# Optimization experiments

Measured on AMD Instinct MI355X. Metric: run time of the kernel, lower is better.

## Reference

```python
import jax, jax.numpy as jnp
import numpy as np

PS = 16            # patch size
STEP = PS - 2      # stride (overlap of 2)
HEADS = 4
DIM = 64
QK = 64
MLP = 128

def _grid(h):
    # static (numpy) row indices of all patch pixels, matching patch_divide's loop
    starts = np.arange(0, h + STEP - PS, STEP)
    tops = np.minimum(starts + PS, h) - PS
    return (tops[:, None] + np.arange(PS)).ravel(), len(starts)

def _div_mask(h):
    # rows/cols covered by two patches get divided by 2 (patch_reverse loops)
    m = np.ones(h, np.float32)
    for i in range(STEP, h + STEP - PS, STEP):
        d = min(i + PS - STEP, h)
        if i < d:
            m[i:d] = 2.0
    return m

def _layernorm(x, g, b):
    mu = x.mean(-1, keepdims=True)
    var = ((x - mu) ** 2).mean(-1, keepdims=True)
    return (x - mu) * jax.lax.rsqrt(var + 1e-5) * g + b

def setup_inputs() -> dict:
    key = jax.random.key(0)
    ks = jax.random.split(key, 8)
    f = lambda k, shp: jax.random.normal(k, shp, jnp.float32) * 0.05
    return {
        "x": jax.random.normal(ks[0], (2, DIM, 226, 226), jnp.float32),
        "ln1_g": jnp.ones((DIM,), jnp.float32), "ln1_b": jnp.zeros((DIM,), jnp.float32),
        "wq": f(ks[1], (DIM, QK)), "wk": f(ks[2], (DIM, QK)), "wv": f(ks[3], (DIM, DIM)),
        "w_proj": f(ks[4], (DIM, DIM)), "b_proj": jnp.zeros((DIM,), jnp.float32),
        "ln2_g": jnp.ones((DIM,), jnp.float32), "ln2_b": jnp.zeros((DIM,), jnp.float32),
        "w_fc1": f(ks[5], (DIM, MLP)), "b_fc1": jnp.zeros((MLP,), jnp.float32),
        "w_dw": f(ks[6], (MLP, 1, 5, 5)), "b_dw": jnp.zeros((MLP,), jnp.float32),
        "w_fc2": f(ks[7], (MLP, DIM)), "b_fc2": jnp.zeros((DIM,), jnp.float32),
    }

def reference(x, ln1_g, ln1_b, wq, wk, wv, w_proj, b_proj,
              ln2_g, ln2_b, w_fc1, b_fc1, w_dw, b_dw, w_fc2, b_fc2):
    b, c, h, w = x.shape
    ri, nh = _grid(h)
    ci, nw = _grid(w)
    n = nh * nw
    # --- patch_divide (vectorized gather of overlapping windows) ---
    p = x[:, :, ri][:, :, :, ci].reshape(b, c, nh, PS, nw, PS)
    t = p.transpose(0, 2, 4, 3, 5, 1).reshape(b * n, PS * PS, c)  # (b n)(h w)c
    # --- PreNorm attention (SDPA default scale = head_dim**-0.5) ---
    y = _layernorm(t, ln1_g, ln1_b)
    dh = QK // HEADS
    q = (y @ wq).reshape(-1, PS * PS, HEADS, dh)
    k = (y @ wk).reshape(-1, PS * PS, HEADS, dh)
    v = (y @ wv).reshape(-1, PS * PS, HEADS, DIM // HEADS)
    logits = jnp.einsum('bqhd,bkhd->bhqk', q, k) * (dh ** -0.5)
    a = jax.nn.softmax(logits, axis=-1)
    o = jnp.einsum('bhqk,bkhd->bqhd', a, v).reshape(-1, PS * PS, DIM)
    t = (o @ w_proj + b_proj) + t
    # --- PreNorm ConvFFN ---
    y = _layernorm(t, ln2_g, ln2_b)
    y = jax.nn.gelu(y @ w_fc1 + b_fc1, approximate=False)
    img = y.reshape(-1, PS, PS, MLP).transpose(0, 3, 1, 2)  # NCHW
    dw = jax.lax.conv_general_dilated(
        img, w_dw, (1, 1), [(2, 2), (2, 2)],
        feature_group_count=MLP,
        dimension_numbers=('NCHW', 'OIHW', 'NCHW')) + b_dw[None, :, None, None]
    dw = jax.nn.gelu(dw, approximate=False).transpose(0, 2, 3, 1).reshape(y.shape)
    y = y + dw
    t = (y @ w_fc2 + b_fc2) + t
    # --- patch_reverse (overlap-add scatter + averaging of double-covered bands) ---
    vals = t.reshape(b, nh, nw, PS, PS, c).transpose(0, 5, 1, 3, 2, 4).reshape(b, c, -1)
    idx = (ri[:, None] * w + ci[None, :]).ravel()
    out = jnp.zeros((b, c, h * w), x.dtype).at[:, :, idx].add(vals)
    out = out.reshape(b, c, h, w) / (_div_mask(h)[:, None] * _div_mask(w)[None, :])
    return out
```

## Files before the change

kernel.cpp:

```cpp
#include <hip/hip_runtime.h>
#include <hip/hip_bf16.h>
#include <math.h>

#define HH 226
#define WW 226
#define HWIMG (226*226)
#define PS 16
#define STP 14
#define TOK 256
#define NPATCH 512
#define NTOK (NPATCH*TOK)
#define OUT_ELEMS (2*64*226*226)

typedef unsigned int u32;
typedef unsigned short u16;
typedef __attribute__((ext_vector_type(8))) short short8;
typedef __attribute__((ext_vector_type(4))) float f32x4;

__device__ __forceinline__ float lo16(u32 u){ return __uint_as_float(u << 16); }
__device__ __forceinline__ float hi16(u32 u){ return __uint_as_float(u & 0xFFFF0000u); }
__device__ __forceinline__ u16 f2bf(float f){
    u32 u = __float_as_uint(f);
    u += 0x7FFFu + ((u >> 16) & 1u);
    return (u16)(u >> 16);
}
__device__ __forceinline__ u32 pack2(float a, float b){
#if defined(__gfx950__) && __has_builtin(__builtin_amdgcn_cvt_pk_bf16_f32)
    auto r = __builtin_amdgcn_cvt_pk_bf16_f32(a, b);
    return *(u32*)&r;
#else
    return (u32)f2bf(a) | ((u32)f2bf(b) << 16);
#endif
}
__device__ __forceinline__ float fexp2(float x){
#if __has_builtin(__builtin_amdgcn_exp2f)
    return __builtin_amdgcn_exp2f(x);
#else
    return exp2f(x);
#endif
}
__device__ __forceinline__ void unpack8(uint4 r, float* d){
    d[0]=lo16(r.x); d[1]=hi16(r.x); d[2]=lo16(r.y); d[3]=hi16(r.y);
    d[4]=lo16(r.z); d[5]=hi16(r.z); d[6]=lo16(r.w); d[7]=hi16(r.w);
}
__device__ __forceinline__ uint4 pack8(const float* a){
    uint4 uu;
    uu.x = pack2(a[0], a[1]);
    uu.y = pack2(a[2], a[3]);
    uu.z = pack2(a[4], a[5]);
    uu.w = pack2(a[6], a[7]);
    return uu;
}
__device__ __forceinline__ float gelu_f(float x){
    return 0.5f * x * (1.0f + erff(x * 0.70710678118654752f));
}

template<int N>
__device__ __forceinline__ void store_bf16(u32* dst, const float* a){
    uint4* p4 = (uint4*)(dst);
    #pragma unroll
    for (int w4 = 0; w4 < N/8; ++w4) p4[w4] = pack8(a + 8*w4);
}

__global__ __launch_bounds__(256, 4) void k0_wt(
    const float* __restrict__ wq, const float* __restrict__ wk,
    const float* __restrict__ wv, u16* __restrict__ wt)
{
    const int i = blockIdx.x*256 + threadIdx.x;
    const int m = i >> 12, rem = i & 4095;
    const int kk = rem >> 6, n = rem & 63;
    const float* w = (m==0 ? wq : (m==1 ? wk : wv));
    wt[m*4096 + n*64 + kk] = f2bf(w[kk*64 + n]);
}

__global__ __launch_bounds__(512, 4) void k1_qkv(
    const float* __restrict__ x, const float* __restrict__ g1, const float* __restrict__ b1,
    const u16* __restrict__ wt,
    float* __restrict__ t_out, u32* __restrict__ qo, u32* __restrict__ ko, u32* __restrict__ vo)
{
    __shared__ u16 ys[256*72];
    __shared__ u32 strip[8][16*34];
    __shared__ float g_s[64], b_s[64];
    const int tid = threadIdx.x;
    if (tid < 64){ g_s[tid]=g1[tid]; b_s[tid]=b1[tid]; }

    const int p = blockIdx.x;
    const int bi = p >> 8, ph = (p >> 4) & 15, pw = p & 15;

    const int tok = tid >> 1, h = tid & 1;
    const int ti = tok >> 4, tj = tok & 15;
    const int r = ph*STP + ti, c = pw*STP + tj;
    const float* xb = x + ((size_t)bi*64 + 32*h)*HWIMG + (size_t)r*WW + c;
    const size_t gtokA = (size_t)p*TOK + tok;
    float* tp = t_out + gtokA*64 + 32*h;

    float v32[32];
    float s1 = 0.f, s2 = 0.f;
    #pragma unroll
    for (int c8 = 0; c8 < 4; ++c8){
        #pragma unroll
        for (int u = 0; u < 8; ++u){
            const float vv = xb[(size_t)(c8*8+u)*HWIMG];
            v32[c8*8+u] = vv;
            s1 += vv; s2 += vv*vv;
        }
        ((float4*)tp)[c8*2]   = make_float4(v32[c8*8+0],v32[c8*8+1],v32[c8*8+2],v32[c8*8+3]);
        ((float4*)tp)[c8*2+1] = make_float4(v32[c8*8+4],v32[c8*8+5],v32[c8*8+6],v32[c8*8+7]);
    }
    s1 += __shfl_xor(s1, 1);
    s2 += __shfl_xor(s2, 1);
    const float mu = s1 * (1.f/64.f);
    const float var = s2 * (1.f/64.f) - mu*mu;
    const float rs = rsqrtf(var + 1e-5f);
    __syncthreads();
    u32* ysw = (u32*)ys;
    #pragma unroll
    for (int i2 = 0; i2 < 16; ++i2){
        const int kk = 32*h + 2*i2;
        const float a0 = (v32[2*i2]  -mu)*rs*g_s[kk]   + b_s[kk];
        const float a1 = (v32[2*i2+1]-mu)*rs*g_s[kk+1] + b_s[kk+1];
        ysw[tok*36 + 16*h + i2] = pack2(a0, a1);
    }
    __syncthreads();

    const int lane = tid & 63;
    const int w8   = tid >> 6;
    const int c15  = lane & 15;
    const int quad = lane >> 4;
    u32* stw = strip[w8];
    const size_t ptok = (size_t)p * TOK;

    for (int mt = 0; mt < 2; ++mt){
        const int T = w8*32 + mt*16;
        short8 af[2];
        #pragma unroll
        for (int kb = 0; kb < 2; ++kb)
            af[kb] = *(const short8*)(ys + (T + c15)*72 + kb*32 + quad*8);

        #pragma unroll
        for (int m = 0; m < 3; ++m){
            short8 bf[2][4];
            #pragma unroll
            for (int kb = 0; kb < 2; ++kb)
                #pragma unroll
                for (int nt = 0; nt < 4; ++nt)
                    bf[kb][nt] = *(const short8*)(wt + m*4096 + (nt*16 + c15)*64 + kb*32 + quad*8);

            f32x4 C[4];
            #pragma unroll
            for (int nt = 0; nt < 4; ++nt) C[nt] = (f32x4){0.f,0.f,0.f,0.f};
            #pragma unroll
            for (int kb = 0; kb < 2; ++kb)
                #pragma unroll
                for (int nt = 0; nt < 4; ++nt)
                    C[nt] = __builtin_amdgcn_mfma_f32_16x16x32_bf16(af[kb], bf[kb][nt], C[nt], 0, 0, 0);

            if (m == 0){
                #pragma unroll
                for (int nt = 0; nt < 4; ++nt)
                    #pragma unroll
                    for (int rr = 0; rr < 4; ++rr)
                        C[nt][rr] *= 0.3606737602222409f;
            }

            #pragma unroll
            for (int nt = 0; nt < 4; ++nt){
                #pragma unroll
                for (int r2 = 0; r2 < 2; ++r2){
                    const float pv0 = __shfl_xor(C[nt][2*r2],   1);
                    const float pv1 = __shfl_xor(C[nt][2*r2+1], 1);
                    u32 wrd; int row;
                    if ((lane & 1) == 0){ wrd = pack2(C[nt][2*r2], pv0);  row = quad*4 + 2*r2; }
                    else                { wrd = pack2(pv1, C[nt][2*r2+1]); row = quad*4 + 2*r2 + 1; }
                    stw[row*34 + nt*8 + (c15 >> 1)] = wrd;
                }
            }

            u32* om = (m==0 ? qo : (m==1 ? ko : vo));
            #pragma unroll
            for (int i = 0; i < 8; ++i){
                const int flat = i*64 + lane;
                const u32 wv = stw[(flat >> 5)*34 + (flat & 31)];
                om[(ptok + T)*32 + flat] = wv;
            }
        }
    }
}

__global__ __launch_bounds__(256, 2) void k2_attn(
    const u16* __restrict__ qg, const u16* __restrict__ kg,
    const u16* __restrict__ vg, u16* __restrict__ og)
{
    __shared__ u16 plds[4][16*280];
    const int tid  = threadIdx.x;
    const int lane = tid & 63;
    const int h    = tid >> 6;
    const int pb   = blockIdx.x;
    const int p    = pb >> 1;
    const int half = pb & 1;
    const int c15  = lane & 15;
    const int quad = lane >> 4;
    const size_t pbase = (size_t)p * TOK * 64;

    short8 kf[16];
    #pragma unroll
    for (int t = 0; t < 16; ++t){
        short8 bf = {0,0,0,0,0,0,0,0};
        if (quad < 2)
            bf = *(const short8*)(kg + pbase + (size_t)(t*16 + c15)*64 + h*16 + quad*8);
        kf[t] = bf;
    }
    short8 vf[8];
    #pragma unroll
    for (int kb = 0; kb < 8; ++kb){
        #pragma unroll
        for (int j = 0; j < 8; ++j)
            vf[kb][j] = (short)vg[pbase + (size_t)(kb*32 + quad*8 + j)*64 + h*16 + c15];
    }
    u16* pw  = &plds[h][0];
    u32* pwq = (u32*)pw + c15*140;

    for (int qi = 0; qi < 8; ++qi){
        const int qt = half*8 + qi;

        short8 qf = {0,0,0,0,0,0,0,0};
        if (quad < 2)
            qf = *(const short8*)(qg + pbase + (size_t)(qt*16 + c15)*64 + h*16 + quad*8);

        f32x4 St[16];
        #pragma unroll
        for (int t = 0; t < 16; ++t){
            f32x4 z = {0.f,0.f,0.f,0.f};
            St[t] = __builtin_amdgcn_mfma_f32_16x16x32_bf16(kf[t], qf, z, 0, 0, 0);
        }

        float rsm[4] = {0.f,0.f,0.f,0.f};
        #pragma unroll
        for (int t = 0; t < 16; ++t){
            #pragma unroll
            for (int r = 0; r < 4; ++r){
                const float pe = fexp2(St[t][r]);
                St[t][r] = pe;
                rsm[r] += pe;
            }
        }
        float s = (rsm[0]+rsm[1]) + (rsm[2]+rsm[3]);
        s += __shfl_xor(s, 16);
        s += __shfl_xor(s, 32);
        const float rinv = __builtin_amdgcn_rcpf(s);
        float rv[4];
        #pragma unroll
        for (int r = 0; r < 4; ++r) rv[r] = __shfl(rinv, quad*4 + r);

        #pragma unroll
        for (int t = 0; t < 16; ++t){
            uint2 wr;
            wr.x = pack2(St[t][0], St[t][1]);
            wr.y = pack2(St[t][2], St[t][3]);
            *(uint2*)(pwq + t*8 + quad*2) = wr;
        }

        f32x4 O0 = {0.f,0.f,0.f,0.f}, O1 = {0.f,0.f,0.f,0.f};
        #pragma unroll
        for (int kb = 0; kb < 4; ++kb){
            const short8 a0 = *(const short8*)(pw + c15*280 + (2*kb)*32 + quad*8);
            const short8 a1 = *(const short8*)(pw + c15*280 + (2*kb+1)*32 + quad*8);
            O0 = __builtin_amdgcn_mfma_f32_16x16x32_bf16(a0, vf[2*kb],   O0, 0, 0, 0);
            O1 = __builtin_amdgcn_mfma_f32_16x16x32_bf16(a1, vf[2*kb+1], O1, 0, 0, 0);
        }

        #pragma unroll
        for (int r = 0; r < 4; ++r){
            const float ov = (O0[r] + O1[r]) * rv[r];
            og[pbase + (size_t)(qt*16 + quad*4 + r)*64 + h*16 + c15] = f2bf(ov);
        }
    }
}

__global__ __launch_bounds__(256, 2) void k3_proj_fc1(
    const u16* __restrict__ og, float* __restrict__ t,
    const float* __restrict__ wp, const float* __restrict__ bp,
    const float* __restrict__ g2, const float* __restrict__ b2,
    const float* __restrict__ wf1, const float* __restrict__ bf1,
    u32* __restrict__ y3)
{
    __shared__ u16 strip[4][16*136];
    __shared__ float bp_s[64], g_s[64], b_s[64], bf_s[128];
    const int tid  = threadIdx.x;
    const int lane = tid & 63;
    const int w    = tid >> 6;
    const int c15  = lane & 15;
    const int quad = lane >> 4;
    if (tid < 64){ bp_s[tid]=bp[tid]; g_s[tid]=g2[tid]; b_s[tid]=b2[tid]; }
    else if (tid >= 128){ const int j = tid - 128; bf_s[j] = bf1[j]; }
    __syncthreads();

    short8 wpf[2][4];
    short8 wff[2][8];
    #pragma unroll
    for (int kb = 0; kb < 2; ++kb){
        #pragma unroll
        for (int nt = 0; nt < 4; ++nt){
            #pragma unroll
            for (int j = 0; j < 8; ++j)
                wpf[kb][nt][j] = (short)f2bf(wp[(kb*32 + quad*8 + j)*64 + nt*16 + c15]);
        }
        #pragma unroll
        for (int nt = 0; nt < 8; ++nt){
            #pragma unroll
            for (int j = 0; j < 8; ++j)
                wff[kb][nt][j] = (short)f2bf(wf1[(kb*32 + quad*8 + j)*128 + nt*16 + c15]);
        }
    }

    const int p = blockIdx.x;
    const size_t pbase = (size_t)p * TOK;
    u16* st = strip[w];
    u32* stw = (u32*)st;

    const float gch[4] = { g_s[0*16+c15], g_s[1*16+c15], g_s[2*16+c15], g_s[3*16+c15] };
    const float bch[4] = { b_s[0*16+c15], b_s[1*16+c15], b_s[2*16+c15], b_s[3*16+c15] };
    const float bpc[4] = { bp_s[0*16+c15], bp_s[1*16+c15], bp_s[2*16+c15], bp_s[3*16+c15] };

    for (int rt = 0; rt < 4; ++rt){
        const int T = w*64 + rt*16;

        short8 af[2];
        #pragma unroll
        for (int kb = 0; kb < 2; ++kb)
            af[kb] = *(const short8*)(og + (pbase + T + c15)*64 + kb*32 + quad*8);

        f32x4 C[4];
        #pragma unroll
        for (int nt = 0; nt < 4; ++nt){
            const float b = bpc[nt];
            C[nt] = (f32x4){b, b, b, b};
        }
        #pragma unroll
        for (int kb = 0; kb < 2; ++kb)
            #pragma unroll
            for (int nt = 0; nt < 4; ++nt)
                C[nt] = __builtin_amdgcn_mfma_f32_16x16x32_bf16(af[kb], wpf[kb][nt], C[nt], 0, 0, 0);

        #pragma unroll
        for (int nt = 0; nt < 4; ++nt){
            #pragma unroll
            for (int r = 0; r < 4; ++r)
                C[nt][r] += t[(pbase + T + quad*4 + r)*64 + nt*16 + c15];
        }
        #pragma unroll
        for (int nt = 0; nt < 4; ++nt){
            #pragma unroll
            for (int r = 0; r < 4; ++r)
                t[(pbase + T + quad*4 + r)*64 + nt*16 + c15] = C[nt][r];
        }

        float rs1[4] = {0,0,0,0}, rs2[4] = {0,0,0,0};
        #pragma unroll
        for (int nt = 0; nt < 4; ++nt)
            #pragma unroll
            for (int r = 0; r < 4; ++r){ rs1[r] += C[nt][r]; rs2[r] += C[nt][r]*C[nt][r]; }
        #pragma unroll
        for (int r = 0; r < 4; ++r){
            rs1[r] += __shfl_xor(rs1[r], 1); rs2[r] += __shfl_xor(rs2[r], 1);
            rs1[r] += __shfl_xor(rs1[r], 2); rs2[r] += __shfl_xor(rs2[r], 2);
            rs1[r] += __shfl_xor(rs1[r], 4); rs2[r] += __shfl_xor(rs2[r], 4);
            rs1[r] += __shfl_xor(rs1[r], 8); rs2[r] += __shfl_xor(rs2[r], 8);
        }
        float muv[4], rsg[4];
        #pragma unroll
        for (int r = 0; r < 4; ++r){
            muv[r] = rs1[r]*(1.f/64.f);
            const float var = rs2[r]*(1.f/64.f) - muv[r]*muv[r];
            rsg[r] = rsqrtf(var + 1e-5f);
        }

        #pragma unroll
        for (int nt = 0; nt < 4; ++nt){
            float yv[4];
            #pragma unroll
            for (int r = 0; r < 4; ++r)
                yv[r] = (C[nt][r]-muv[r])*rsg[r]*gch[nt] + bch[nt];
            #pragma unroll
            for (int r2 = 0; r2 < 2; ++r2){
                const float pv0 = __shfl_xor(yv[2*r2],   1);
                const float pv1 = __shfl_xor(yv[2*r2+1], 1);
                u32 wrd; int row;
                if ((lane & 1) == 0){ wrd = pack2(yv[2*r2], pv0);  row = quad*4 + 2*r2; }
                else                { wrd = pack2(pv1, yv[2*r2+1]); row = quad*4 + 2*r2 + 1; }
                *(u32*)(st + row*136 + nt*16 + (c15 & ~1)) = wrd;
            }
        }

        short8 pa[2];
        #pragma unroll
        for (int kb = 0; kb < 2; ++kb)
            pa[kb] = *(const short8*)(st + c15*136 + kb*32 + quad*8);

        f32x4 F[8];
        #pragma unroll
        for (int nt = 0; nt < 8; ++nt){
            const float b = bf_s[nt*16 + c15];
            F[nt] = (f32x4){b, b, b, b};
        }
        #pragma unroll
        for (int kb = 0; kb < 2; ++kb)
            #pragma unroll
            for (int nt = 0; nt < 8; ++nt)
                F[nt] = __builtin_amdgcn_mfma_f32_16x16x32_bf16(pa[kb], wff[kb][nt], F[nt], 0, 0, 0);

        #pragma unroll
        for (int nt = 0; nt < 8; ++nt)
            #pragma unroll
            for (int r = 0; r < 4; ++r)
                F[nt][r] = gelu_f(F[nt][r]);

        #pragma unroll
        for (int nt = 0; nt < 8; ++nt){
            #pragma unroll
            for (int r2 = 0; r2 < 2; ++r2){
                const float pv0 = __shfl_xor(F[nt][2*r2],   1);
                const float pv1 = __shfl_xor(F[nt][2*r2+1], 1);
                u32 wrd; int row;
                if ((lane & 1) == 0){ wrd = pack2(F[nt][2*r2], pv0);  row = quad*4 + 2*r2; }
                else                { wrd = pack2(pv1, F[nt][2*r2+1]); row = quad*4 + 2*r2 + 1; }
                *(u32*)(st + row*136 + nt*16 + (c15 & ~1)) = wrd;
            }
        }
        #pragma unroll
        for (int i = 0; i < 16; ++i){
            const u32 wv = stw[i*68 + lane];
            y3[(pbase + T + i)*64 + lane] = wv;
        }
    }
}

__global__ __launch_bounds__(256, 2) void k4a_dwconv(
    u32* y3, const float* __restrict__ wdw, const float* __restrict__ bdw)
{
    __shared__ u32 ys[400*33];
    __shared__ float wdwT[25*64];
    __shared__ float bdw_s[64];
    const int tid = threadIdx.x;
    const int p = blockIdx.x;
    const int ti = tid >> 4, tj = tid & 15;
    const int stok = (ti+2)*20 + (tj+2);
    const size_t gtok = (size_t)p*TOK + tid;
    for (int i = tid; i < 13200; i += 256) ys[i] = 0u;
    for (int half = 0; half < 2; ++half){
        __syncthreads();
        for (int i = tid; i < 1600; i += 256){
            int chh = i/25, tap = i%25;
            wdwT[tap*64+chh] = wdw[(half*64+chh)*25 + tap];
        }
        if (tid < 64) bdw_s[tid] = bdw[half*64+tid];
        {
            const uint4* gp = (const uint4*)(y3 + gtok*64 + half*32);
            #pragma unroll
            for (int w = 0; w < 8; ++w){
                uint4 rr = gp[w];
                ys[stok*33 + w*4+0]=rr.x; ys[stok*33 + w*4+1]=rr.y;
                ys[stok*33 + w*4+2]=rr.z; ys[stok*33 + w*4+3]=rr.w;
            }
        }
        __syncthreads();
        const int base = stok*33;
        for (int ch2 = 0; ch2 < 32; ++ch2){
            float a0 = bdw_s[2*ch2], a1 = bdw_s[2*ch2+1];
            #pragma unroll
            for (int tap = 0; tap < 25; ++tap){
                const int di = tap/5, dj = tap%5;
                const int woff = ((di-2)*20 + (dj-2))*33;
                const u32 w0 = ys[base + woff + ch2];
                a0 += lo16(w0)*wdwT[tap*64+2*ch2];
                a1 += hi16(w0)*wdwT[tap*64+2*ch2+1];
            }
            const u32 own = ys[base + ch2];
            const float o0 = lo16(own) + gelu_f(a0);
            const float o1 = hi16(own) + gelu_f(a1);
            y3[gtok*64 + half*32 + ch2] = pack2(o0, o1);
        }
    }
}

__global__ __launch_bounds__(256, 2) void k4b_fc2(
    const u16* __restrict__ y3h, const float* __restrict__ t2,
    const float* __restrict__ wf2, const float* __restrict__ bf2,
    float* __restrict__ t3)
{
    const int tid  = threadIdx.x;
    const int lane = tid & 63;
    const int w    = tid >> 6;
    const int c15  = lane & 15;
    const int quad = lane >> 4;

    short8 wf[4][4];
    #pragma unroll
    for (int kb = 0; kb < 4; ++kb)
        #pragma unroll
        for (int nt = 0; nt < 4; ++nt)
            #pragma unroll
            for (int j = 0; j < 8; ++j)
                wf[kb][nt][j] = (short)f2bf(wf2[(kb*32 + quad*8 + j)*64 + nt*16 + c15]);

    float bcc[4];
    #pragma unroll
    for (int nt = 0; nt < 4; ++nt) bcc[nt] = bf2[nt*16 + c15];

    const int p = blockIdx.x;
    const size_t pbase = (size_t)p * TOK;
    float* t3p = t3 + (size_t)p * 16384;

    for (int rt = 0; rt < 4; ++rt){
        const int T = w*64 + rt*16;

        short8 af[4];
        #pragma unroll
        for (int kb = 0; kb < 4; ++kb)
            af[kb] = *(const short8*)(y3h + (pbase + T + c15)*128 + kb*32 + quad*8);

        f32x4 C[4];
        #pragma unroll
        for (int nt = 0; nt < 4; ++nt){
            const float b = bcc[nt];
            C[nt] = (f32x4){b, b, b, b};
        }
        #pragma unroll
        for (int kb = 0; kb < 4; ++kb)
            #pragma unroll
            for (int nt = 0; nt < 4; ++nt)
                C[nt] = __builtin_amdgcn_mfma_f32_16x16x32_bf16(af[kb], wf[kb][nt], C[nt], 0, 0, 0);

        #pragma unroll
        for (int nt = 0; nt < 4; ++nt)
            #pragma unroll
            for (int r = 0; r < 4; ++r)
                C[nt][r] += t2[(pbase + T + quad*4 + r)*64 + nt*16 + c15];

        #pragma unroll
        for (int nt = 0; nt < 4; ++nt)
            #pragma unroll
            for (int r = 0; r < 4; ++r)
                t3p[(nt*16 + c15)*256 + T + quad*4 + r] = C[nt][r];
    }
}

__global__ __launch_bounds__(256, 4) void k5_reverse(
    const float* __restrict__ t3, float* __restrict__ out)
{
    const int e = blockIdx.x*256 + threadIdx.x;
    if (e >= OUT_ELEMS) return;
    const int c = e % WW;
    int tmp = e / WW;
    const int r = tmp % HH;
    tmp /= HH;
    const int ch = tmp & 63;
    const int b = tmp >> 6;
    int pr = r/14; if (pr > 15) pr = 15;
    int pc = c/14; if (pc > 15) pc = 15;
    const int ra = r - pr*14, ca = c - pc*14;
    const int rb = ra + 14, cb = ca + 14;
    const bool hr = (pr >= 1) && (rb < 16);
    const bool hc = (pc >= 1) && (cb < 16);
    #define T3IDX(PH,PC,I,J) (((((b*16+(PH))*16+(PC))*64 + ch) << 8) + (I)*16 + (J))
    float s = t3[T3IDX(pr,pc,ra,ca)];
    if (hr)       s += t3[T3IDX(pr-1,pc,  rb,ca)];
    if (hc)       s += t3[T3IDX(pr,  pc-1,ra,cb)];
    if (hr && hc) s += t3[T3IDX(pr-1,pc-1,rb,cb)];
    const float f = (hr ? 0.5f : 1.f) * (hc ? 0.5f : 1.f);
    out[e] = s * f;
    #undef T3IDX
}

extern "C" void kernel_launch(void* const* d_in, const int* in_sizes, int n_in,
                              void* d_out, int out_size, void* d_ws, size_t ws_size,
                              hipStream_t stream)
{
    const float* x    = (const float*)d_in[0];
    const float* g1   = (const float*)d_in[1];
    const float* b1   = (const float*)d_in[2];
    const float* wq   = (const float*)d_in[3];
    const float* wk   = (const float*)d_in[4];
    const float* wv   = (const float*)d_in[5];
    const float* wp   = (const float*)d_in[6];
    const float* bp   = (const float*)d_in[7];
    const float* g2   = (const float*)d_in[8];
    const float* b2   = (const float*)d_in[9];
    const float* wf1  = (const float*)d_in[10];
    const float* bf1  = (const float*)d_in[11];
    const float* wdw  = (const float*)d_in[12];
    const float* bdw  = (const float*)d_in[13];
    const float* wf2  = (const float*)d_in[14];
    const float* bf2  = (const float*)d_in[15];

    char* ws = (char*)d_ws;
    float* t  = (float*)(ws);
    u32* q    = (u32*)(ws + 33554432);
    u32* k    = (u32*)(ws + 50331648);
    u32* v    = (u32*)(ws + 67108864);
    float* t3 = (float*)(ws + 50331648);
    u32* y3   = (u32*)(ws + 83886080);
    u16* wt   = (u16*)d_out;
    float* out = (float*)d_out;

    k0_wt      <<<48,        256, 0, stream>>>(wq, wk, wv, wt);
    k1_qkv     <<<NPATCH,    512, 0, stream>>>(x, g1, b1, wt, t, q, k, v);
    k2_attn    <<<NPATCH*2,  256, 0, stream>>>((const u16*)q, (const u16*)k, (const u16*)v, (u16*)q);
    k3_proj_fc1<<<NPATCH,    256, 0, stream>>>((const u16*)q, t, wp, bp, g2, b2, wf1, bf1, y3);
    k4a_dwconv <<<NPATCH,    256, 0, stream>>>(y3, wdw, bdw);
    k4b_fc2    <<<NPATCH,    256, 0, stream>>>((const u16*)y3, t, wf2, bf2, t3);
    k5_reverse <<<25538,     256, 0, stream>>>(t3, out);
}
```

Baseline: 348.7 us.

## Restructure depthwise conv to per-thread channel columns with sliding register window

The depthwise 5x5 conv kernel now assigns each thread a channel pair and two image columns instead of one token looping over all channels. Filter weights and bias are held in registers rather than shared memory. A 5x5 register window slides down the column, so each shared-memory value is loaded once per row step instead of 25 times. This adds register pressure (about 50 weight floats plus 25 window words), which may lower occupancy. Output stores also become strided by token.

```diff
diff --git a/kernel.cpp b/kernel.cpp
--- a/kernel.cpp
+++ b/kernel.cpp
@@ -439,46 +439,68 @@
     u32* y3, const float* __restrict__ wdw, const float* __restrict__ bdw)
 {
     __shared__ u32 ys[400*33];
-    __shared__ float wdwT[25*64];
-    __shared__ float bdw_s[64];
     const int tid = threadIdx.x;
     const int p = blockIdx.x;
-    const int ti = tid >> 4, tj = tid & 15;
-    const int stok = (ti+2)*20 + (tj+2);
-    const size_t gtok = (size_t)p*TOK + tid;
+    const int ch2 = tid & 31;
+    const int cg  = tid >> 5;
+    const size_t ptok = (size_t)p * TOK;
+
+    const int fti = tid >> 4, ftj = tid & 15;
+    const int fstok = (fti+2)*20 + (ftj+2);
+
     for (int i = tid; i < 13200; i += 256) ys[i] = 0u;
+
     for (int half = 0; half < 2; ++half){
         __syncthreads();
-        for (int i = tid; i < 1600; i += 256){
-            int chh = i/25, tap = i%25;
-            wdwT[tap*64+chh] = wdw[(half*64+chh)*25 + tap];
-        }
-        if (tid < 64) bdw_s[tid] = bdw[half*64+tid];
         {
-            const uint4* gp = (const uint4*)(y3 + gtok*64 + half*32);
+            const uint4* gp = (const uint4*)(y3 + (ptok + tid)*64 + half*32);
             #pragma unroll
             for (int w = 0; w < 8; ++w){
                 uint4 rr = gp[w];
-                ys[stok*33 + w*4+0]=rr.x; ys[stok*33 + w*4+1]=rr.y;
-                ys[stok*33 + w*4+2]=rr.z; ys[stok*33 + w*4+3]=rr.w;
-            }
-        }
+                ys[fstok*33 + w*4+0]=rr.x; ys[fstok*33 + w*4+1]=rr.y;
+                ys[fstok*33 + w*4+2]=rr.z; ys[fstok*33 + w*4+3]=rr.w;
+            }
+        }
+        float wA[25], wB[25];
+        #pragma unroll
+        for (int tap = 0; tap < 25; ++tap){
+            wA[tap] = wdw[(half*64 + 2*ch2+0)*25 + tap];
+            wB[tap] = wdw[(half*64 + 2*ch2+1)*25 + tap];
+        }
+        const float bA = bdw[half*64 + 2*ch2+0];
+        const float bB = bdw[half*64 + 2*ch2+1];
         __syncthreads();
-        const int base = stok*33;
-        for (int ch2 = 0; ch2 < 32; ++ch2){
-            float a0 = bdw_s[2*ch2], a1 = bdw_s[2*ch2+1];
-            #pragma unroll
-            for (int tap = 0; tap < 25; ++tap){
-                const int di = tap/5, dj = tap%5;
-                const int woff = ((di-2)*20 + (dj-2))*33;
-                const u32 w0 = ys[base + woff + ch2];
-                a0 += lo16(w0)*wdwT[tap*64+2*ch2];
-                a1 += hi16(w0)*wdwT[tap*64+2*ch2+1];
-            }
-            const u32 own = ys[base + ch2];
-            const float o0 = lo16(own) + gelu_f(a0);
-            const float o1 = hi16(own) + gelu_f(a1);
-            y3[gtok*64 + half*32 + ch2] = pack2(o0, o1);
+
+        #pragma unroll
+        for (int cc = 0; cc < 2; ++cc){
+            const int c  = cg*2 + cc;
+            const int hc = c + 2;
+            u32 win[5][5];
+            #pragma unroll
+            for (int r = 0; r < 4; ++r)
+                #pragma unroll
+                for (int j = 0; j < 5; ++j)
+                    win[r][j] = ys[(r*20 + hc-2+j)*33 + ch2];
+            #pragma unroll
+            for (int row = 0; row < 16; ++row){
+                #pragma unroll
+                for (int j = 0; j < 5; ++j)
+                    win[(row+4)%5][j] = ys[((row+4)*20 + hc-2+j)*33 + ch2];
+                float a0 = bA, a1 = bB;
+                #pragma unroll
+                for (int di = 0; di < 5; ++di){
+                    #pragma unroll
+                    for (int dj = 0; dj < 5; ++dj){
+                        const u32 v = win[(row+di)%5][dj];
+                        a0 += lo16(v)*wA[di*5+dj];
+                        a1 += hi16(v)*wB[di*5+dj];
+                    }
+                }
+                const u32 own = win[(row+2)%5][2];
+                const float o0 = lo16(own) + gelu_f(a0);
+                const float o1 = hi16(own) + gelu_f(a1);
+                y3[(ptok + row*16 + c)*64 + half*32 + ch2] = pack2(o0, o1);
+            }
         }
     }
 }
```

New measurement: 313.1 us. -10.2%, faster.
